# Kernel optimization log

Measured on AMD Instinct MI355X. Metric: run time of the kernel, lower is better.

The kernel has to match this reference:

```python
import jax, jax.numpy as jnp
import numpy as np

# Static configuration (matches init_kwargs)
NW, WH, WW, SH, SW = 1024, 8, 8, 2, 2
EMBED, NH = 192, 6
HD = EMBED // NH            # 32
NP = WH * WW                # 64 patches per window
S2 = SH * SW                # 4 shuffle groups
L = NP * S2                 # 256 tokens per window
NWM = 64                    # number of mask windows
SCALE = HD ** (-0.5) / SH   # head_dim**-0.5 / shuffle
EPS = 1e-5


def _rel_pos_index():
    # Swin-style relative position index for an (8,8) window.
    coords = np.stack(np.meshgrid(np.arange(WH), np.arange(WW), indexing='ij')).reshape(2, -1)
    rel = (coords[:, :, None] - coords[:, None, :]).transpose(1, 2, 0)  # (64,64,2)
    rel[..., 0] += WH - 1
    rel[..., 0] *= 2 * WW - 1
    rel[..., 1] += WW - 1
    return jnp.asarray(rel.sum(-1).reshape(-1))  # (4096,) values in [0, 225)

REL_IDX = _rel_pos_index()


def _group(x):
    # 'nw (wh sh ww sw) ch -> nw (wh ww) (sh sw) ch'
    return x.reshape(NW, WH, SH, WW, SW, EMBED).transpose(0, 1, 3, 2, 4, 5).reshape(NW, NP, S2, EMBED)


def _ungroup(x):
    # 'nw (wh ww) (sh sw) ch -> nw (wh sh ww sw) ch'
    return x.reshape(NW, WH, WW, SH, SW, EMBED).transpose(0, 1, 3, 2, 4, 5).reshape(NW, L, EMBED)


def _ln(x, w, b):
    # LayerNorm over the last two dims [shuffle**2, embed_dim]
    mu = x.mean(axis=(-2, -1), keepdims=True)
    var = x.var(axis=(-2, -1), keepdims=True)
    return (x - mu) * jax.lax.rsqrt(var + EPS) * w + b


def _heads(x):
    # 'nw np s2 (nh hd) -> nw nh np s2 hd'
    return x.reshape(NW, NP, S2, NH, HD).transpose(0, 3, 1, 2, 4)


def setup_inputs() -> dict:
    key = jax.random.key(0)
    ks = jax.random.split(key, 7)
    inp = {
        'query': jax.random.normal(ks[0], (NW, L, EMBED), jnp.float32),
        'key': jax.random.normal(ks[1], (NW, L, EMBED), jnp.float32),
        'value': jax.random.normal(ks[2], (NW, L, EMBED), jnp.float32),
        'mask': jax.random.normal(ks[3], (NWM, NP, NP), jnp.float32),
        'ln_q_w': jnp.ones((S2, EMBED), jnp.float32),
        'ln_q_b': jnp.zeros((S2, EMBED), jnp.float32),
        'ln_k_w': jnp.ones((S2, EMBED), jnp.float32),
        'ln_k_b': jnp.zeros((S2, EMBED), jnp.float32),
        'ln_v_w': jnp.ones((S2, EMBED), jnp.float32),
        'ln_v_b': jnp.zeros((S2, EMBED), jnp.float32),
        'bias_table': 0.02 * jax.random.normal(ks[4], ((2 * WH - 1) * (2 * WW - 1), NH), jnp.float32),
        'proj_w': 0.02 * jax.random.normal(ks[5], (EMBED, EMBED), jnp.float32),  # nn.Linear weight (out,in)
    }
    return inp


def reference(query, key, value, mask, ln_q_w, ln_q_b, ln_k_w, ln_k_b, ln_v_w, ln_v_b, bias_table, proj_w):
    q = _heads(_ln(_group(query), ln_q_w, ln_q_b)) * SCALE   # (nw,nh,np,s2,hd)
    k = _heads(_ln(_group(key), ln_k_w, ln_k_b))
    v = _heads(_ln(_group(value), ln_v_w, ln_v_b))

    attn = jnp.einsum('whqsc,whksc->whqk', q, k)              # (nw,nh,np,np)

    bias = bias_table[REL_IDX].reshape(NP, NP, NH).transpose(2, 0, 1)  # (nh,np,np)
    attn = attn + bias[None]

    b = NW // NWM
    attn = (attn.reshape(b, NWM, NH, NP, NP) + mask[None, :, None]).reshape(NW, NH, NP, NP)

    attn = jax.nn.softmax(attn, axis=-1)

    out = jnp.einsum('whqk,whksc->whqsc', attn, v)            # (nw,nh,np,s2,hd)
    out = out.transpose(0, 2, 3, 1, 4).reshape(NW, NP, S2, EMBED)
    out = _ungroup(out)                                       # (nw, L, embed)
    return out @ proj_w.T
```

## Files before the change

### kernel.cpp

```cpp
#include <hip/hip_runtime.h>

#define NWIN 1024
#define LTOK 256
#define EMB  192
#define NPAT 64
#define NHEAD 6
#define HDIM 32
#define SCALE 0.08838834764831845f
#define LN_EPS 1e-5f

typedef float f32x4 __attribute__((ext_vector_type(4)));
typedef short s16x8 __attribute__((ext_vector_type(8)));

#define OFF_KH  0
#define OFF_VT  16384
#define OFF_PB  32768
#define OFF_SB  40960
#define OFF_OB  58368
#define OFF_ST  91136
#define OFF_BH  92672
#define SMEM_BYTES 93696

__device__ __forceinline__ unsigned short f2bf(float f) {
    unsigned u = __float_as_uint(f);
    u += 0x7fffu + ((u >> 16) & 1u);
    return (unsigned short)(u >> 16);
}

__device__ __forceinline__ int tok_of(int p, int s) {
    return ((p >> 3) << 5) + ((s >> 1) << 4) + ((p & 7) << 1) + (s & 1);
}

__device__ __forceinline__ f32x4 mfma16(s16x8 a, s16x8 b, f32x4 c) {
    return __builtin_amdgcn_mfma_f32_16x16x32_bf16(a, b, c, 0, 0, 0);
}

__device__ __forceinline__ s16x8 ln_pack8r(const float* v, float mu, float rs,
                                           const float* __restrict__ wl,
                                           const float* __restrict__ bl,
                                           float scale) {
    f32x4 w0 = *(const f32x4*)wl;
    f32x4 w1 = *(const f32x4*)(wl + 4);
    f32x4 c0 = *(const f32x4*)bl;
    f32x4 c1 = *(const f32x4*)(bl + 4);
    s16x8 r;
    r[0] = (short)f2bf(((v[0]-mu)*rs*w0[0] + c0[0])*scale);
    r[1] = (short)f2bf(((v[1]-mu)*rs*w0[1] + c0[1])*scale);
    r[2] = (short)f2bf(((v[2]-mu)*rs*w0[2] + c0[2])*scale);
    r[3] = (short)f2bf(((v[3]-mu)*rs*w0[3] + c0[3])*scale);
    r[4] = (short)f2bf(((v[4]-mu)*rs*w1[0] + c1[0])*scale);
    r[5] = (short)f2bf(((v[5]-mu)*rs*w1[1] + c1[1])*scale);
    r[6] = (short)f2bf(((v[6]-mu)*rs*w1[2] + c1[2])*scale);
    r[7] = (short)f2bf(((v[7]-mu)*rs*w1[3] + c1[3])*scale);
    return r;
}

__device__ __forceinline__ void ln_f8r(const float* v, float mu, float rs,
                                       const float* __restrict__ wl,
                                       const float* __restrict__ bl,
                                       float* o) {
    f32x4 w0 = *(const f32x4*)wl;
    f32x4 w1 = *(const f32x4*)(wl + 4);
    f32x4 c0 = *(const f32x4*)bl;
    f32x4 c1 = *(const f32x4*)(bl + 4);
    o[0] = (v[0]-mu)*rs*w0[0] + c0[0];
    o[1] = (v[1]-mu)*rs*w0[1] + c0[1];
    o[2] = (v[2]-mu)*rs*w0[2] + c0[2];
    o[3] = (v[3]-mu)*rs*w0[3] + c0[3];
    o[4] = (v[4]-mu)*rs*w1[0] + c1[0];
    o[5] = (v[5]-mu)*rs*w1[1] + c1[1];
    o[6] = (v[6]-mu)*rs*w1[2] + c1[2];
    o[7] = (v[7]-mu)*rs*w1[3] + c1[3];
}

__device__ __forceinline__ void load_KV(const float* __restrict__ k_g,
                                        const float* __restrict__ v_g,
                                        size_t wbase, int tid, int hh,
                                        float kpre[2][8], float vpre[2][8]) {
    #pragma unroll
    for (int i = 0; i < 2; ++i) {
        int c = i*512 + tid;
        int p = c >> 4, s = (c >> 2) & 3, cb = c & 3;
        int t = tok_of(p, s);
        const float* kp = k_g + wbase + t*EMB + hh*HDIM + cb*8;
        const float* vp = v_g + wbase + t*EMB + hh*HDIM + cb*8;
        *(f32x4*)&kpre[i][0] = *(const f32x4*)kp;
        *(f32x4*)&kpre[i][4] = *(const f32x4*)(kp + 4);
        *(f32x4*)&vpre[i][0] = *(const f32x4*)vp;
        *(f32x4*)&vpre[i][4] = *(const f32x4*)(vp + 4);
    }
}

__device__ __forceinline__ void stage_K(char* smem, int tid, int hh,
                                        const float kpre[2][8], const float* stats,
                                        const float* __restrict__ lnkw,
                                        const float* __restrict__ lnkb) {
    const float* muk = stats + 128; const float* rsk = stats + 192;
    #pragma unroll
    for (int i = 0; i < 2; ++i) {
        int c = i*512 + tid;
        int p = c >> 4, s = (c >> 2) & 3, cb = c & 3;
        int chb = hh*HDIM + cb*8;
        s16x8 kk = ln_pack8r(kpre[i], muk[p], rsk[p],
                             lnkw + s*EMB + chb, lnkb + s*EMB + chb, 1.0f);
        *(s16x8*)(smem + OFF_KH + p*256 + ((s*64 + cb*16) ^ ((p & 7) << 4))) = kk;
    }
}

__device__ __forceinline__ void stage_V(char* smem, int tid, int hh,
                                        const float vpre[2][8], const float* stats,
                                        const float* __restrict__ lnvw,
                                        const float* __restrict__ lnvb) {
    const float* muv = stats + 256; const float* rsv = stats + 320;
    #pragma unroll
    for (int i = 0; i < 2; ++i) {
        int c = i*512 + tid;
        int p = c >> 4, s = (c >> 2) & 3, cb = c & 3;
        int chb = hh*HDIM + cb*8;
        float vn[8];
        ln_f8r(vpre[i], muv[p], rsv[p], lnvw + s*EMB + chb, lnvb + s*EMB + chb, vn);
        #pragma unroll
        for (int j = 0; j < 8; ++j) {
            int sc = s*32 + cb*8 + j;
            *(unsigned short*)(smem + OFF_VT + sc*128 + ((p*2) ^ ((sc & 7) << 4)))
                = f2bf(vn[j]);
        }
    }
}

__device__ __forceinline__ void load_Q(const float* __restrict__ q_g, size_t wbase,
                                       int pr, int cb, int hh, float qpre[4][8]) {
    #pragma unroll
    for (int ks = 0; ks < 4; ++ks) {
        int t = tok_of(pr, ks);
        const float* qp = q_g + wbase + t*EMB + hh*HDIM + cb*8;
        *(f32x4*)&qpre[ks][0] = *(const f32x4*)qp;
        *(f32x4*)&qpre[ks][4] = *(const f32x4*)(qp + 4);
    }
}


__global__ __launch_bounds__(512, 2) void dwa_attn_kernel(
    const float* __restrict__ q_g, const float* __restrict__ k_g,
    const float* __restrict__ v_g, const float* __restrict__ mask_g,
    const float* __restrict__ lnqw, const float* __restrict__ lnqb,
    const float* __restrict__ lnkw, const float* __restrict__ lnkb,
    const float* __restrict__ lnvw, const float* __restrict__ lnvb,
    const float* __restrict__ btab, float* __restrict__ out_g)
{
    __shared__ __align__(16) char smem[SMEM_BYTES];

    const int tid  = threadIdx.x;
    const int lane = tid & 63;
    const int wv   = tid >> 6;
    const int win  = blockIdx.x;
    const size_t wbase = (size_t)win * LTOK * EMB;
    char* preb = (char*)out_g + (size_t)win * 196608;

    float* stats = (float*)(smem + OFF_ST);
    float* muq = stats;       float* rsq = stats + 64;
    float* biash = (float*)(smem + OFF_BH);

    const int mwin = win & 63;
    const float* mask_w = mask_g + (size_t)mwin * NPAT * NPAT;

    const int sm_qr = tid >> 3, sm_j = tid & 7;
    f32x4 mk0 = *(const f32x4*)(mask_w + sm_qr*64 + sm_j*8);
    f32x4 mk1 = *(const f32x4*)(mask_w + sm_qr*64 + sm_j*8 + 4);

    {
        float* part = (float*)(smem + OFF_SB);
        const int t = tid >> 1, half = tid & 1;
        const f32x4* qp = (const f32x4*)(q_g + wbase + t*EMB + half*96);
        const f32x4* kp = (const f32x4*)(k_g + wbase + t*EMB + half*96);
        const f32x4* vp = (const f32x4*)(v_g + wbase + t*EMB + half*96);
        float s1q=0.f,s2q=0.f,s1k=0.f,s2k=0.f,s1v=0.f,s2v=0.f;
        #pragma unroll 4
        for (int i = 0; i < 24; ++i) {
            f32x4 a = qp[i];
            s1q += a[0]+a[1]+a[2]+a[3];
            s2q += a[0]*a[0]+a[1]*a[1]+a[2]*a[2]+a[3]*a[3];
            f32x4 b = kp[i];
            s1k += b[0]+b[1]+b[2]+b[3];
            s2k += b[0]*b[0]+b[1]*b[1]+b[2]*b[2]+b[3]*b[3];
            f32x4 c = vp[i];
            s1v += c[0]+c[1]+c[2]+c[3];
            s2v += c[0]*c[0]+c[1]*c[1]+c[2]*c[2]+c[3]*c[3];
        }
        float* pp = part + (t*2 + half)*6;
        pp[0]=s1q; pp[1]=s2q; pp[2]=s1k; pp[3]=s2k; pp[4]=s1v; pp[5]=s2v;
        __syncthreads();
        if (tid < NPAT) {
            float S[6] = {0.f,0.f,0.f,0.f,0.f,0.f};
            #pragma unroll
            for (int s = 0; s < 4; ++s) {
                int tt = tok_of(tid, s);
                const float* pr_ = part + tt*12;
                #pragma unroll
                for (int x = 0; x < 6; ++x) S[x] += pr_[x] + pr_[6 + x];
            }
            #pragma unroll
            for (int x = 0; x < 3; ++x) {
                float mu  = S[2*x] * (1.f/768.f);
                float var = S[2*x+1] * (1.f/768.f) - mu*mu;
                stats[x*128 + tid]      = mu;
                stats[x*128 + 64 + tid] = rsqrtf(var + LN_EPS);
            }
        }
        __syncthreads();
    }

    const int mstrip = wv >> 1;
    const int pr = mstrip*16 + (lane & 15);
    const int cb = lane >> 4;

    float qpre[4][8];
    {
        float kpre[2][8], vpre[2][8];
        load_KV(k_g, v_g, wbase, tid, 0, kpre, vpre);
        load_Q(q_g, wbase, pr, cb, 0, qpre);
        if (tid < 225) biash[tid] = btab[tid * NHEAD];
        stage_K(smem, tid, 0, kpre, stats, lnkw, lnkb);
        stage_V(smem, tid, 0, vpre, stats, lnvw, lnvb);
    }
    __syncthreads();

    for (int h = 0; h < NHEAD; ++h) {
        float kpre[2][8], vpre[2][8]; float breg = 0.f;
        if (h < NHEAD-1) {
            load_KV(k_g, v_g, wbase, tid, h+1, kpre, vpre);
            if (tid < 225) breg = btab[tid * NHEAD + h + 1];
        }

        {
            int nhalf = wv & 1;
            float mu = muq[pr], rs = rsq[pr];
            f32x4 acc0 = {0.f,0.f,0.f,0.f};
            f32x4 acc1 = {0.f,0.f,0.f,0.f};
            #pragma unroll
            for (int ks = 0; ks < 4; ++ks) {
                int chb = h*HDIM + cb*8;
                s16x8 af = ln_pack8r(qpre[ks], mu, rs,
                                     lnqw + ks*EMB + chb, lnqb + ks*EMB + chb, SCALE);
                {
                    int row = (nhalf*2 + 0)*16 + (lane & 15);
                    s16x8 bf = *(const s16x8*)(smem + OFF_KH + row*256 +
                                  ((ks*64 + cb*16) ^ ((row & 7) << 4)));
                    acc0 = mfma16(af, bf, acc0);
                }
                {
                    int row = (nhalf*2 + 1)*16 + (lane & 15);
                    s16x8 bf = *(const s16x8*)(smem + OFF_KH + row*256 +
                                  ((ks*64 + cb*16) ^ ((row & 7) << 4)));
                    acc1 = mfma16(af, bf, acc1);
                }
            }
            float* Sb = (float*)(smem + OFF_SB);
            #pragma unroll
            for (int r = 0; r < 4; ++r) {
                int qr = mstrip*16 + (lane >> 4)*4 + r;
                Sb[qr*68 + (nhalf*2+0)*16 + (lane & 15)] = acc0[r];
                Sb[qr*68 + (nhalf*2+1)*16 + (lane & 15)] = acc1[r];
            }
        }
        __syncthreads();

        {
            const float* Sb = (const float*)(smem + OFF_SB);
            f32x4 s0 = *(const f32x4*)(Sb + sm_qr*68 + sm_j*8);
            f32x4 s1 = *(const f32x4*)(Sb + sm_qr*68 + sm_j*8 + 4);
            int qh = sm_qr >> 3, qw = sm_qr & 7;
            float vals[8];
            #pragma unroll
            for (int jj = 0; jj < 8; ++jj) {
                int kc = sm_j*8 + jj;
                int idx = (qh - (kc >> 3) + 7)*15 + (qw - (kc & 7) + 7);
                vals[jj] = (jj < 4 ? s0[jj] : s1[jj-4]) +
                           (jj < 4 ? mk0[jj] : mk1[jj-4]) + biash[idx];
            }
            float mx = vals[0];
            #pragma unroll
            for (int jj = 1; jj < 8; ++jj) mx = fmaxf(mx, vals[jj]);
            mx = fmaxf(mx, __shfl_xor(mx, 1));
            mx = fmaxf(mx, __shfl_xor(mx, 2));
            mx = fmaxf(mx, __shfl_xor(mx, 4));
            float sum = 0.f;
            #pragma unroll
            for (int jj = 0; jj < 8; ++jj) { vals[jj] = __expf(vals[jj] - mx); sum += vals[jj]; }
            sum += __shfl_xor(sum, 1);
            sum += __shfl_xor(sum, 2);
            sum += __shfl_xor(sum, 4);
            float rinv = 1.f / sum;
            s16x8 pv;
            #pragma unroll
            for (int jj = 0; jj < 8; ++jj) pv[jj] = (short)f2bf(vals[jj] * rinv);
            *(s16x8*)(smem + OFF_PB + sm_qr*128 + ((sm_j*16) ^ ((sm_qr & 7) << 4))) = pv;
        }
        if (h < NHEAD-1) {
            stage_K(smem, tid, h+1, kpre, stats, lnkw, lnkb);
            load_Q(q_g, wbase, pr, cb, h+1, qpre);
        }
        __syncthreads();

        {
            int m = wv >> 1, nset = wv & 1;
            int prow = m*16 + (lane & 15);
            s16x8 ap0 = *(const s16x8*)(smem + OFF_PB + prow*128 +
                          ((0*64 + cb*16) ^ ((prow & 7) << 4)));
            s16x8 ap1 = *(const s16x8*)(smem + OFF_PB + prow*128 +
                          ((1*64 + cb*16) ^ ((prow & 7) << 4)));
            #pragma unroll
            for (int i = 0; i < 4; ++i) {
                int nt = nset*4 + i;
                int brow = nt*16 + (lane & 15);
                f32x4 acc = {0.f,0.f,0.f,0.f};
                s16x8 bf0 = *(const s16x8*)(smem + OFF_VT + brow*128 +
                              ((0*64 + cb*16) ^ ((brow & 7) << 4)));
                s16x8 bf1 = *(const s16x8*)(smem + OFF_VT + brow*128 +
                              ((1*64 + cb*16) ^ ((brow & 7) << 4)));
                acc = mfma16(ap0, bf0, acc);
                acc = mfma16(ap1, bf1, acc);
                int sc = nt*16 + (lane & 15);
                #pragma unroll
                for (int r = 0; r < 4; ++r) {
                    int qp = m*16 + (lane >> 4)*4 + r;
                    *(unsigned short*)(smem + OFF_OB + qp*512 +
                        (((h & 1)*256 + sc*2) ^ ((qp & 7) << 4))) = f2bf(acc[r]);
                }
            }
        }
        __syncthreads();

        if (h & 1) {
            int hpair = h >> 1;
            #pragma unroll
            for (int i = 0; i < 4; ++i) {
                int c = i*512 + tid;
                int t = c >> 3, ch8 = c & 7;
                int hp = ch8 >> 2, c2b = ch8 & 3;
                int qp = ((t >> 5) << 3) | ((t >> 1) & 7);
                int s  = (((t >> 4) & 1) << 1) | (t & 1);
                s16x8 v = *(const s16x8*)(smem + OFF_OB + qp*512 +
                              ((hp*256 + s*64 + c2b*16) ^ ((qp & 7) << 4)));
                *(s16x8*)(preb + (size_t)t*768 + 384 + hpair*128 + hp*64 + c2b*16) = v;
            }
        }
        if (h < NHEAD-1) {
            stage_V(smem, tid, h+1, vpre, stats, lnvw, lnvb);
            if (tid < 225) biash[tid] = breg;
        }
        __syncthreads();
    }
}

__global__ __launch_bounds__(256, 2) void dwa_proj_kernel(
    const float* __restrict__ pw, float* __restrict__ out_g)
{
    __shared__ __align__(16) char smem[73728];

    const int tid  = threadIdx.x;
    const int lane = tid & 63;
    const int wv   = tid >> 6;
    const int w    = blockIdx.x;
    const char* preb = (const char*)out_g + (size_t)w * 196608;
    const int cb = lane >> 4;

    s16x8 af[4][6];
    #pragma unroll
    for (int si = 0; si < 4; ++si) {
        int strip = wv*4 + si;
        int arow = strip*16 + (lane & 15);
        #pragma unroll
        for (int ks = 0; ks < 6; ++ks)
            af[si][ks] = *(const s16x8*)(preb + (size_t)arow*768 + 384 + ks*64 + cb*16);
    }

    #pragma unroll 2
    for (int i = 0; i < 18; ++i) {
        int c = i*256 + tid;
        int orow = c / 24, cb8 = c % 24;
        const float* wp = pw + (size_t)orow*EMB + cb8*8;
        f32x4 a = *(const f32x4*)wp;
        f32x4 b = *(const f32x4*)(wp + 4);
        s16x8 w8;
        w8[0] = (short)f2bf(a[0]); w8[1] = (short)f2bf(a[1]);
        w8[2] = (short)f2bf(a[2]); w8[3] = (short)f2bf(a[3]);
        w8[4] = (short)f2bf(b[0]); w8[5] = (short)f2bf(b[1]);
        w8[6] = (short)f2bf(b[2]); w8[7] = (short)f2bf(b[3]);
        *(s16x8*)(smem + orow*384 + ((cb8*16) ^ ((orow & 7) << 4))) = w8;
    }
    __syncthreads();

    #pragma unroll
    for (int si = 0; si < 4; ++si) {
        int strip = wv*4 + si;
        #pragma unroll
        for (int nt = 0; nt < 12; ++nt) {
            int orow = nt*16 + (lane & 15);
            f32x4 acc = {0.f,0.f,0.f,0.f};
            #pragma unroll
            for (int ks = 0; ks < 6; ++ks) {
                s16x8 bf = *(const s16x8*)(smem + orow*384 +
                              ((ks*64 + cb*16) ^ ((orow & 7) << 4)));
                acc = mfma16(af[si][ks], bf, acc);
            }
            #pragma unroll
            for (int r = 0; r < 4; ++r) {
                int trow = strip*16 + (lane >> 4)*4 + r;
                out_g[(size_t)w*49152 + trow*EMB + nt*16 + (lane & 15)] = acc[r];
            }
        }
    }
}

extern "C" void kernel_launch(void* const* d_in, const int* in_sizes, int n_in,
                              void* d_out, int out_size, void* d_ws, size_t ws_size,
                              hipStream_t stream) {
    (void)in_sizes; (void)n_in; (void)out_size; (void)d_ws; (void)ws_size;
    dwa_attn_kernel<<<dim3(NWIN), dim3(512), 0, stream>>>(
        (const float*)d_in[0],  (const float*)d_in[1],  (const float*)d_in[2],
        (const float*)d_in[3],  (const float*)d_in[4],  (const float*)d_in[5],
        (const float*)d_in[6],  (const float*)d_in[7],  (const float*)d_in[8],
        (const float*)d_in[9],  (const float*)d_in[10],
        (float*)d_out);
    dwa_proj_kernel<<<dim3(NWIN), dim3(256), 0, stream>>>(
        (const float*)d_in[11], (float*)d_out);
}
```

Baseline: 427.5 us.

## Fuse softmax into QK MFMA epilogue and cut shared memory and barriers

Computes bias, mask and softmax directly on the QK^T MFMA accumulators, using wave shuffles plus a small cross-wave max/sum exchange, instead of storing scores to a shared scratch buffer and re-reading them. This drops the score buffer, which lowers shared memory use, and the launch bounds ask for higher occupancy. It also removes one barrier per head by moving bias staging and V staging, reorganises K/V loads so each thread handles one patch, changes the output swizzle, and adds s_setprio around MFMA sections. The risk is register pressure under the tighter launch bound, plus extra shuffles and scalar LDS writes.

After: 619.1 us. 1.45x slower.

```diff
diff --git a/kernel.cpp b/kernel.cpp
--- a/kernel.cpp
+++ b/kernel.cpp
@@ -15,11 +15,11 @@
 #define OFF_KH  0
 #define OFF_VT  16384
 #define OFF_PB  32768
-#define OFF_SB  40960
-#define OFF_OB  58368
-#define OFF_ST  91136
-#define OFF_BH  92672
-#define SMEM_BYTES 93696
+#define OFF_OB  40960
+#define OFF_ST  73728
+#define OFF_BH  75264
+#define OFF_HB  76288
+#define SMEM_BYTES 77312
 
 __device__ __forceinline__ unsigned short f2bf(float f) {
     unsigned u = __float_as_uint(f);
@@ -73,21 +73,17 @@
     o[7] = (v[7]-mu)*rs*w1[3] + c1[3];
 }
 
-__device__ __forceinline__ void load_KV(const float* __restrict__ k_g,
-                                        const float* __restrict__ v_g,
-                                        size_t wbase, int tid, int hh,
-                                        float kpre[2][8], float vpre[2][8]) {
+__device__ __forceinline__ void load_T8(const float* __restrict__ g, size_t wbase,
+                                        int tid, int hh, float pre[2][8]) {
+    int p = tid & 63;
     #pragma unroll
     for (int i = 0; i < 2; ++i) {
-        int c = i*512 + tid;
-        int p = c >> 4, s = (c >> 2) & 3, cb = c & 3;
+        int scb = (tid >> 6) * 2 + i;
+        int s = scb >> 2, cbx = scb & 3;
         int t = tok_of(p, s);
-        const float* kp = k_g + wbase + t*EMB + hh*HDIM + cb*8;
-        const float* vp = v_g + wbase + t*EMB + hh*HDIM + cb*8;
-        *(f32x4*)&kpre[i][0] = *(const f32x4*)kp;
-        *(f32x4*)&kpre[i][4] = *(const f32x4*)(kp + 4);
-        *(f32x4*)&vpre[i][0] = *(const f32x4*)vp;
-        *(f32x4*)&vpre[i][4] = *(const f32x4*)(vp + 4);
+        const float* gp = g + wbase + t*EMB + hh*HDIM + cbx*8;
+        *(f32x4*)&pre[i][0] = *(const f32x4*)gp;
+        *(f32x4*)&pre[i][4] = *(const f32x4*)(gp + 4);
     }
 }
 
@@ -96,14 +92,15 @@
                                         const float* __restrict__ lnkw,
                                         const float* __restrict__ lnkb) {
     const float* muk = stats + 128; const float* rsk = stats + 192;
+    int p = tid & 63;
     #pragma unroll
     for (int i = 0; i < 2; ++i) {
-        int c = i*512 + tid;
-        int p = c >> 4, s = (c >> 2) & 3, cb = c & 3;
-        int chb = hh*HDIM + cb*8;
+        int scb = (tid >> 6) * 2 + i;
+        int s = scb >> 2, cbx = scb & 3;
+        int chb = hh*HDIM + cbx*8;
         s16x8 kk = ln_pack8r(kpre[i], muk[p], rsk[p],
                              lnkw + s*EMB + chb, lnkb + s*EMB + chb, 1.0f);
-        *(s16x8*)(smem + OFF_KH + p*256 + ((s*64 + cb*16) ^ ((p & 7) << 4))) = kk;
+        *(s16x8*)(smem + OFF_KH + p*256 + ((scb*16) ^ ((p & 7) << 4))) = kk;
     }
 }
 
@@ -112,16 +109,17 @@
                                         const float* __restrict__ lnvw,
                                         const float* __restrict__ lnvb) {
     const float* muv = stats + 256; const float* rsv = stats + 320;
+    int p = tid & 63;
     #pragma unroll
     for (int i = 0; i < 2; ++i) {
-        int c = i*512 + tid;
-        int p = c >> 4, s = (c >> 2) & 3, cb = c & 3;
-        int chb = hh*HDIM + cb*8;
+        int scb = (tid >> 6) * 2 + i;
+        int s = scb >> 2, cbx = scb & 3;
+        int chb = hh*HDIM + cbx*8;
         float vn[8];
         ln_f8r(vpre[i], muv[p], rsv[p], lnvw + s*EMB + chb, lnvb + s*EMB + chb, vn);
         #pragma unroll
         for (int j = 0; j < 8; ++j) {
-            int sc = s*32 + cb*8 + j;
+            int sc = scb*8 + j;
             *(unsigned short*)(smem + OFF_VT + sc*128 + ((p*2) ^ ((sc & 7) << 4)))
                 = f2bf(vn[j]);
         }
@@ -140,7 +138,7 @@
 }
 
 
-__global__ __launch_bounds__(512, 2) void dwa_attn_kernel(
+__global__ __launch_bounds__(512, 4) void dwa_attn_kernel(
     const float* __restrict__ q_g, const float* __restrict__ k_g,
     const float* __restrict__ v_g, const float* __restrict__ mask_g,
     const float* __restrict__ lnqw, const float* __restrict__ lnqb,
@@ -160,16 +158,32 @@
     float* stats = (float*)(smem + OFF_ST);
     float* muq = stats;       float* rsq = stats + 64;
     float* biash = (float*)(smem + OFF_BH);
-
-    const int mwin = win & 63;
-    const float* mask_w = mask_g + (size_t)mwin * NPAT * NPAT;
-
-    const int sm_qr = tid >> 3, sm_j = tid & 7;
-    f32x4 mk0 = *(const f32x4*)(mask_w + sm_qr*64 + sm_j*8);
-    f32x4 mk1 = *(const f32x4*)(mask_w + sm_qr*64 + sm_j*8 + 4);
-
+    float2* HB = (float2*)(smem + OFF_HB);
+
+    const int mstrip = wv >> 1, nhalf = wv & 1;
+    const int l15 = lane & 15, l4 = lane >> 4;
+    const int pr = mstrip*16 + l15;
+    const int cb = l4;
+
+    const float* mask_w = mask_g + (size_t)(win & 63) * NPAT * NPAT;
+    const int kc0 = nhalf*32 + l15, kc1 = kc0 + 16;
+    float mm0[4], mm1[4];
+    int idx0[4], idx1[4], qrr[4];
     {
-        float* part = (float*)(smem + OFF_SB);
+        int kh0 = kc0 >> 3, kw0 = kc0 & 7, kh1 = kc1 >> 3, kw1 = kc1 & 7;
+        #pragma unroll
+        for (int r = 0; r < 4; ++r) {
+            int qr = mstrip*16 + l4*4 + r;
+            qrr[r] = qr;
+            mm0[r] = mask_w[qr*64 + kc0];
+            mm1[r] = mask_w[qr*64 + kc1];
+            idx0[r] = ((qr>>3) - kh0 + 7)*15 + ((qr&7) - kw0 + 7);
+            idx1[r] = ((qr>>3) - kh1 + 7)*15 + ((qr&7) - kw1 + 7);
+        }
+    }
+
+    {
+        float* part = (float*)(smem + OFF_OB);
         const int t = tid >> 1, half = tid & 1;
         const f32x4* qp = (const f32x4*)(q_g + wbase + t*EMB + half*96);
         const f32x4* kp = (const f32x4*)(k_g + wbase + t*EMB + half*96);
@@ -210,124 +224,122 @@
         __syncthreads();
     }
 
-    const int mstrip = wv >> 1;
-    const int pr = mstrip*16 + (lane & 15);
-    const int cb = lane >> 4;
-
-    float qpre[4][8];
-    {
-        float kpre[2][8], vpre[2][8];
-        load_KV(k_g, v_g, wbase, tid, 0, kpre, vpre);
-        load_Q(q_g, wbase, pr, cb, 0, qpre);
-        if (tid < 225) biash[tid] = btab[tid * NHEAD];
-        stage_K(smem, tid, 0, kpre, stats, lnkw, lnkb);
-        stage_V(smem, tid, 0, vpre, stats, lnvw, lnvb);
-    }
+    float kpre[2][8], vpre[2][8], qpre[4][8];
+    float breg;
+    load_T8(k_g, wbase, tid, 0, kpre);
+    load_T8(v_g, wbase, tid, 0, vpre);
+    load_Q(q_g, wbase, pr, cb, 0, qpre);
+    breg = (tid < 225) ? btab[tid * NHEAD] : 0.f;
+    stage_K(smem, tid, 0, kpre, stats, lnkw, lnkb);
+    stage_V(smem, tid, 0, vpre, stats, lnvw, lnvb);
+    if (tid < 225) biash[tid] = breg;
     __syncthreads();
 
     for (int h = 0; h < NHEAD; ++h) {
-        float kpre[2][8], vpre[2][8]; float breg = 0.f;
-        if (h < NHEAD-1) {
-            load_KV(k_g, v_g, wbase, tid, h+1, kpre, vpre);
-            if (tid < 225) breg = btab[tid * NHEAD + h + 1];
-        }
-
+        const bool pf = (h < NHEAD-1);
+        if (pf) {
+            load_T8(k_g, wbase, tid, h+1, kpre);
+            load_T8(v_g, wbase, tid, h+1, vpre);
+            breg = (tid < 225) ? btab[tid*NHEAD + h + 1] : 0.f;
+        }
+
+        float e0[4], e1[4], mrow[4], srow[4];
         {
-            int nhalf = wv & 1;
             float mu = muq[pr], rs = rsq[pr];
             f32x4 acc0 = {0.f,0.f,0.f,0.f};
             f32x4 acc1 = {0.f,0.f,0.f,0.f};
+            __builtin_amdgcn_s_setprio(1);
             #pragma unroll
             for (int ks = 0; ks < 4; ++ks) {
                 int chb = h*HDIM + cb*8;
                 s16x8 af = ln_pack8r(qpre[ks], mu, rs,
                                      lnqw + ks*EMB + chb, lnqb + ks*EMB + chb, SCALE);
                 {
-                    int row = (nhalf*2 + 0)*16 + (lane & 15);
+                    int row = nhalf*32 + l15;
                     s16x8 bf = *(const s16x8*)(smem + OFF_KH + row*256 +
                                   ((ks*64 + cb*16) ^ ((row & 7) << 4)));
                     acc0 = mfma16(af, bf, acc0);
                 }
                 {
-                    int row = (nhalf*2 + 1)*16 + (lane & 15);
+                    int row = nhalf*32 + 16 + l15;
                     s16x8 bf = *(const s16x8*)(smem + OFF_KH + row*256 +
                                   ((ks*64 + cb*16) ^ ((row & 7) << 4)));
                     acc1 = mfma16(af, bf, acc1);
                 }
             }
-            float* Sb = (float*)(smem + OFF_SB);
+            __builtin_amdgcn_s_setprio(0);
             #pragma unroll
             for (int r = 0; r < 4; ++r) {
-                int qr = mstrip*16 + (lane >> 4)*4 + r;
-                Sb[qr*68 + (nhalf*2+0)*16 + (lane & 15)] = acc0[r];
-                Sb[qr*68 + (nhalf*2+1)*16 + (lane & 15)] = acc1[r];
+                float L0 = acc0[r] + mm0[r] + biash[idx0[r]];
+                float L1 = acc1[r] + mm1[r] + biash[idx1[r]];
+                float m = fmaxf(L0, L1);
+                m = fmaxf(m, __shfl_xor(m, 1));
+                m = fmaxf(m, __shfl_xor(m, 2));
+                m = fmaxf(m, __shfl_xor(m, 4));
+                m = fmaxf(m, __shfl_xor(m, 8));
+                float a = __expf(L0 - m), b = __expf(L1 - m);
+                float s = a + b;
+                s += __shfl_xor(s, 1);
+                s += __shfl_xor(s, 2);
+                s += __shfl_xor(s, 4);
+                s += __shfl_xor(s, 8);
+                e0[r] = a; e1[r] = b; mrow[r] = m; srow[r] = s;
+            }
+            if (l15 == 0) {
+                #pragma unroll
+                for (int r = 0; r < 4; ++r) {
+                    float2 v; v.x = mrow[r]; v.y = srow[r];
+                    HB[qrr[r]*2 + nhalf] = v;
+                }
             }
         }
         __syncthreads();
 
-        {
-            const float* Sb = (const float*)(smem + OFF_SB);
-            f32x4 s0 = *(const f32x4*)(Sb + sm_qr*68 + sm_j*8);
-            f32x4 s1 = *(const f32x4*)(Sb + sm_qr*68 + sm_j*8 + 4);
-            int qh = sm_qr >> 3, qw = sm_qr & 7;
-            float vals[8];
-            #pragma unroll
-            for (int jj = 0; jj < 8; ++jj) {
-                int kc = sm_j*8 + jj;
-                int idx = (qh - (kc >> 3) + 7)*15 + (qw - (kc & 7) + 7);
-                vals[jj] = (jj < 4 ? s0[jj] : s1[jj-4]) +
-                           (jj < 4 ? mk0[jj] : mk1[jj-4]) + biash[idx];
-            }
-            float mx = vals[0];
-            #pragma unroll
-            for (int jj = 1; jj < 8; ++jj) mx = fmaxf(mx, vals[jj]);
-            mx = fmaxf(mx, __shfl_xor(mx, 1));
-            mx = fmaxf(mx, __shfl_xor(mx, 2));
-            mx = fmaxf(mx, __shfl_xor(mx, 4));
-            float sum = 0.f;
-            #pragma unroll
-            for (int jj = 0; jj < 8; ++jj) { vals[jj] = __expf(vals[jj] - mx); sum += vals[jj]; }
-            sum += __shfl_xor(sum, 1);
-            sum += __shfl_xor(sum, 2);
-            sum += __shfl_xor(sum, 4);
-            float rinv = 1.f / sum;
-            s16x8 pv;
-            #pragma unroll
-            for (int jj = 0; jj < 8; ++jj) pv[jj] = (short)f2bf(vals[jj] * rinv);
-            *(s16x8*)(smem + OFF_PB + sm_qr*128 + ((sm_j*16) ^ ((sm_qr & 7) << 4))) = pv;
-        }
-        if (h < NHEAD-1) {
+        if (pf) {
             stage_K(smem, tid, h+1, kpre, stats, lnkw, lnkb);
             load_Q(q_g, wbase, pr, cb, h+1, qpre);
+            if (tid < 225) biash[tid] = breg;
+        }
+        #pragma unroll
+        for (int r = 0; r < 4; ++r) {
+            int qr = qrr[r];
+            float2 ha = HB[qr*2 + 0], hb = HB[qr*2 + 1];
+            float M = fmaxf(ha.x, hb.x);
+            float tot = ha.y*__expf(ha.x - M) + hb.y*__expf(hb.x - M);
+            float f = __expf(mrow[r] - M) / tot;
+            unsigned short p0 = f2bf(e0[r]*f);
+            unsigned short p1 = f2bf(e1[r]*f);
+            *(unsigned short*)(smem + OFF_PB + qr*128 + ((kc0*2) ^ ((qr & 7) << 4))) = p0;
+            *(unsigned short*)(smem + OFF_PB + qr*128 + ((kc1*2) ^ ((qr & 7) << 4))) = p1;
         }
         __syncthreads();
 
         {
-            int m = wv >> 1, nset = wv & 1;
-            int prow = m*16 + (lane & 15);
-            s16x8 ap0 = *(const s16x8*)(smem + OFF_PB + prow*128 +
-                          ((0*64 + cb*16) ^ ((prow & 7) << 4)));
-            s16x8 ap1 = *(const s16x8*)(smem + OFF_PB + prow*128 +
-                          ((1*64 + cb*16) ^ ((prow & 7) << 4)));
+            s16x8 ap0 = *(const s16x8*)(smem + OFF_PB + pr*128 +
+                          ((cb*16) ^ ((pr & 7) << 4)));
+            s16x8 ap1 = *(const s16x8*)(smem + OFF_PB + pr*128 +
+                          ((64 + cb*16) ^ ((pr & 7) << 4)));
+            __builtin_amdgcn_s_setprio(1);
             #pragma unroll
             for (int i = 0; i < 4; ++i) {
-                int nt = nset*4 + i;
-                int brow = nt*16 + (lane & 15);
+                int nt = nhalf*4 + i;
+                int brow = nt*16 + l15;
                 f32x4 acc = {0.f,0.f,0.f,0.f};
                 s16x8 bf0 = *(const s16x8*)(smem + OFF_VT + brow*128 +
-                              ((0*64 + cb*16) ^ ((brow & 7) << 4)));
+                              ((cb*16) ^ ((brow & 7) << 4)));
                 s16x8 bf1 = *(const s16x8*)(smem + OFF_VT + brow*128 +
-                              ((1*64 + cb*16) ^ ((brow & 7) << 4)));
+                              ((64 + cb*16) ^ ((brow & 7) << 4)));
                 acc = mfma16(ap0, bf0, acc);
                 acc = mfma16(ap1, bf1, acc);
-                int sc = nt*16 + (lane & 15);
+                int sc = nt*16 + l15;
                 #pragma unroll
                 for (int r = 0; r < 4; ++r) {
-                    int qp = m*16 + (lane >> 4)*4 + r;
+                    int qp = mstrip*16 + l4*4 + r;
                     *(unsigned short*)(smem + OFF_OB + qp*512 +
-                        (((h & 1)*256 + sc*2) ^ ((qp & 7) << 4))) = f2bf(acc[r]);
+                        (((h & 1)*256 + sc*2) ^ (((qp >> 2) & 3) << 5))) = f2bf(acc[r]);
                 }
             }
+            __builtin_amdgcn_s_setprio(0);
         }
         __syncthreads();
 
@@ -341,15 +353,11 @@
                 int qp = ((t >> 5) << 3) | ((t >> 1) & 7);
                 int s  = (((t >> 4) & 1) << 1) | (t & 1);
                 s16x8 v = *(const s16x8*)(smem + OFF_OB + qp*512 +
-                              ((hp*256 + s*64 + c2b*16) ^ ((qp & 7) << 4)));
+                              ((hp*256 + s*64 + c2b*16) ^ (((qp >> 2) & 3) << 5)));
                 *(s16x8*)(preb + (size_t)t*768 + 384 + hpair*128 + hp*64 + c2b*16) = v;
             }
         }
-        if (h < NHEAD-1) {
-            stage_V(smem, tid, h+1, vpre, stats, lnvw, lnvb);
-            if (tid < 225) biash[tid] = breg;
-        }
-        __syncthreads();
+        if (pf) stage_V(smem, tid, h+1, vpre, stats, lnvw, lnvb);
     }
 }
 
```
